# Kernel tuning notes

Measured on AMD Instinct MI355X. Metric: run time of the kernel, lower is better.

## Reference

```python
import jax, jax.numpy as jnp
import numpy as np

C = 64

def setup_inputs() -> dict:
    key = jax.random.key(0)
    ks = jax.random.split(key, 8)
    B, H, W = 4, 64, 64
    s = 1.0 / np.sqrt(C)
    return {
        "x": jax.random.normal(ks[0], (B, C, H, W), dtype=jnp.float32),
        "ln_g": jnp.ones((C,), jnp.float32),
        "ln_b": jnp.zeros((C,), jnp.float32),
        "wq": jax.random.normal(ks[1], (C, C), jnp.float32) * s,
        "bq": jnp.zeros((C,), jnp.float32),
        "wk": jax.random.normal(ks[2], (C, 1, 3, 3), jnp.float32) / 3.0,
        "bk": jnp.zeros((C,), jnp.float32),
        "wv": jax.random.normal(ks[3], (C, 1, 3, 3), jnp.float32) / 3.0,
        "bv": jnp.zeros((C,), jnp.float32),
        "wo": jax.random.normal(ks[4], (C, C), jnp.float32) * s,
        "bo": jnp.zeros((C,), jnp.float32),
    }

def _dwconv3x3(x, w, b):
    # depthwise 3x3, padding=1, groups=C; x: (B,C,H,W), w: (C,1,3,3)
    y = jax.lax.conv_general_dilated(
        x, w, window_strides=(1, 1), padding="SAME",
        feature_group_count=x.shape[1],
        dimension_numbers=("NCHW", "OIHW", "NCHW"))
    return y + b[None, :, None, None]

def reference(x, ln_g, ln_b, wq, bq, wk, bk, wv, bv, wo, bo):
    B, Cc, H, W = x.shape
    scale = jnp.sqrt(jnp.asarray(Cc, x.dtype))
    # LayerNorm over channel dim (torch LayerNorm([C]) on (B,H,W,C))
    mu = jnp.mean(x, axis=1, keepdims=True)
    var = jnp.mean(jnp.square(x - mu), axis=1, keepdims=True)
    xn = (x - mu) / jnp.sqrt(var + 1e-5)
    xn = xn * ln_g[None, :, None, None] + ln_b[None, :, None, None]
    # projections
    q = jnp.einsum("oc,bchw->bohw", wq, xn) + bq[None, :, None, None]
    k = _dwconv3x3(xn, wk, bk)
    v = _dwconv3x3(xn, wv, bv)
    HW = H * W
    qf = q.reshape(B, Cc, HW)  # (B,C,N)
    kf = k.reshape(B, Cc, HW)
    vf = v.reshape(B, Cc, HW)
    # attn[b,i,j] = sum_c q[b,c,i] k[b,c,j] / sqrt(C)
    attn = jnp.einsum("bci,bcj->bij", qf, kf) / scale
    attn = jax.nn.softmax(attn, axis=-1)
    # out[b,c,i] = sum_j attn[b,i,j] v[b,c,j]
    out = jnp.einsum("bij,bcj->bci", attn, vf).reshape(B, Cc, H, W)
    out = jnp.einsum("oc,bchw->bohw", wo, out) + bo[None, :, None, None]
    return out + x
```

## Files before the change

kernel.cpp:

```cpp
#include <hip/hip_runtime.h>
#include <stdint.h>

typedef __attribute__((ext_vector_type(8))) short short8;
typedef __attribute__((ext_vector_type(4))) float f32x4;

#define MFMA16(A, B, C) __builtin_amdgcn_mfma_f32_16x16x32_bf16(A, B, C, 0, 0, 0)

__device__ __forceinline__ short f2bf(float f) {
    uint32_t u = __float_as_uint(f);
    u = (u + 0x7fffu + ((u >> 16) & 1u)) >> 16;
    return (short)u;
}
__device__ __forceinline__ uint32_t pk_bf_trunc(float a, float b) {
    return __builtin_amdgcn_perm(__float_as_uint(b), __float_as_uint(a), 0x07060302u);
}
union PFU { uint32_t u[4]; short8 s; };

__device__ __forceinline__ void async_cp16(void* lds, const void* gm) {
    __builtin_amdgcn_global_load_lds(
        (const __attribute__((address_space(1))) unsigned int*)gm,
        (__attribute__((address_space(3))) unsigned int*)lds,
        16, 0, 0);
}

__device__ __forceinline__ int swz(int row, int col) {
    return row * 64 + ((((col >> 3) ^ (row & 7)) << 3) | (col & 7));
}
__device__ __forceinline__ int pimap(int j) {
    return ((j >> 5) << 5) + (((j >> 2) & 3) << 3) + (((j >> 4) & 1) << 2) + (j & 3);
}

__device__ __forceinline__ short8 ldg_f8_bf(const float* __restrict__ p) {
    float4 a = *(const float4*)p;
    float4 b = *(const float4*)(p + 4);
    short8 r;
    r[0] = f2bf(a.x); r[1] = f2bf(a.y); r[2] = f2bf(a.z); r[3] = f2bf(a.w);
    r[4] = f2bf(b.x); r[5] = f2bf(b.y); r[6] = f2bf(b.z); r[7] = f2bf(b.w);
    return r;
}

__global__ __launch_bounds__(512, 2) void k_lnqkv(
    const float* __restrict__ xg, const float* __restrict__ lng, const float* __restrict__ lnb,
    const float* __restrict__ wq, const float* __restrict__ bq,
    const float* __restrict__ wkg, const float* __restrict__ bk,
    const float* __restrict__ wvg, const float* __restrict__ bv,
    short* __restrict__ Qt, short* __restrict__ KVg)
{
    const int t    = threadIdx.x;
    const int wv   = t >> 6;
    const int lane = t & 63;
    const int l15  = lane & 15;
    const int quad = lane >> 4;
    const int h    = blockIdx.x;
    const int b    = blockIdx.y;
    const int w    = t & 63;
    const int g    = t >> 6;

    __shared__ float xl[3 * 64 * 66];
    __shared__ float sfu[3072];
    __shared__ float wkl[576], wvl[576], bkl[64], bvl[64];
    __shared__ float muL[192], rsL[192];

    float rv[24];
    float s0 = 0.f, s1 = 0.f, s2 = 0.f, q0 = 0.f, q1 = 0.f, q2 = 0.f;
    #pragma unroll
    for (int k = 0; k < 24; ++k) {
        const int dy = k >> 3, c = g + 8 * (k & 7);
        const int hh = h + dy - 1;
        float v = 0.f;
        if (hh >= 0 && hh < 64) v = xg[((b * 64 + c) * 64 + hh) * 64 + w];
        rv[k] = v;
        if (k < 8)       { s0 += v; q0 = fmaf(v, v, q0); }
        else if (k < 16) { s1 += v; q1 = fmaf(v, v, q1); }
        else             { s2 += v; q2 = fmaf(v, v, q2); }
    }
    float lngv[8], lnbv[8];
    #pragma unroll
    for (int j = 0; j < 8; ++j) { lngv[j] = lng[g + 8 * j]; lnbv[j] = lnb[g + 8 * j]; }
    for (int idx = t; idx < 576; idx += 512) { wkl[idx] = wkg[idx]; wvl[idx] = wvg[idx]; }
    if (t < 64) { bkl[t] = bk[t]; bvl[t] = bv[t]; }
    #pragma unroll
    for (int k = 0; k < 24; ++k)
        xl[((k >> 3) * 64 + g + 8 * (k & 7)) * 66 + w] = rv[k];
    sfu[(0 * 8 + g) * 64 + w] = s0; sfu[(1 * 8 + g) * 64 + w] = s1; sfu[(2 * 8 + g) * 64 + w] = s2;
    sfu[1536 + (0 * 8 + g) * 64 + w] = q0; sfu[1536 + (1 * 8 + g) * 64 + w] = q1; sfu[1536 + (2 * 8 + g) * 64 + w] = q2;
    __syncthreads();

    if (t < 192) {
        int dy = t >> 6, ww = t & 63;
        float S = 0.f, SS = 0.f;
        #pragma unroll
        for (int gg = 0; gg < 8; ++gg) {
            S  += sfu[(dy * 8 + gg) * 64 + ww];
            SS += sfu[1536 + (dy * 8 + gg) * 64 + ww];
        }
        float mu  = S * (1.f / 64.f);
        float var = SS * (1.f / 64.f) - mu * mu;
        muL[t] = mu;
        rsL[t] = rsqrtf(var + 1e-5f);
    }
    __syncthreads();

    short* xnt = (short*)sfu;
    {
        float mua = muL[w], rsa = rsL[w];
        float mub = muL[64 + w], rsb = rsL[64 + w];
        float muc = muL[128 + w], rsc = rsL[128 + w];
        #pragma unroll
        for (int k = 0; k < 24; ++k) {
            int dy = k >> 3, c = g + 8 * (k & 7);
            int hh = h + dy - 1;
            float mu = (k < 8) ? mua : (k < 16) ? mub : muc;
            float rs = (k < 8) ? rsa : (k < 16) ? rsb : rsc;
            float v = (rv[k] - mu) * rs * lngv[k & 7] + lnbv[k & 7];
            if (hh < 0 || hh >= 64) v = 0.f;
            xl[(dy * 64 + c) * 66 + w] = v;
            if (dy == 1) xnt[w * 72 + c] = f2bf(v);
        }
    }
    __syncthreads();

    {
        const int tile = wv >> 1, half = wv & 1;
        short8 af[2];
        #pragma unroll
        for (int kc = 0; kc < 2; ++kc)
            af[kc] = *(const short8*)&xnt[(tile * 16 + l15) * 72 + kc * 32 + quad * 8];
        f32x4 acc[2];
        acc[0] = (f32x4){0.f, 0.f, 0.f, 0.f};
        acc[1] = (f32x4){0.f, 0.f, 0.f, 0.f};
        #pragma unroll
        for (int kc = 0; kc < 2; ++kc) {
            #pragma unroll
            for (int ntl = 0; ntl < 2; ++ntl) {
                int nt = half * 2 + ntl;
                short8 bf = ldg_f8_bf(&wq[(nt * 16 + l15) * 64 + kc * 32 + quad * 8]);
                acc[ntl] = MFMA16(af[kc], bf, acc[ntl]);
            }
        }
        const float c1 = 0.18033688011112042f;
        #pragma unroll
        for (int ntl = 0; ntl < 2; ++ntl) {
            int o = (half * 2 + ntl) * 16 + l15;
            float bqv = bq[o];
            #pragma unroll
            for (int r = 0; r < 4; ++r) {
                int ww = tile * 16 + quad * 4 + r;
                Qt[((b * 4096 + h * 64 + ww) << 6) + o] = f2bf((acc[ntl][r] + bqv) * c1);
            }
        }
    }
    __syncthreads();

    short* vt = (short*)sfu;
    {
        int c  = t & 63;
        int w0 = wv << 3;
        float wk9[9], wv9[9];
        #pragma unroll
        for (int q = 0; q < 9; ++q) { wk9[q] = wkl[c * 9 + q]; wv9[q] = wvl[c * 9 + q]; }
        float acck[8], accv[8];
        #pragma unroll
        for (int j = 0; j < 8; ++j) { acck[j] = bkl[c]; accv[j] = bvl[c]; }
        #pragma unroll
        for (int dy = 0; dy < 3; ++dy) {
            const float* row = &xl[(dy * 64 + c) * 66];
            float r[10];
            r[0] = (w0 == 0) ? 0.f : row[w0 - 1];
            #pragma unroll
            for (int j2 = 0; j2 < 4; ++j2) {
                float2 p2 = *(const float2*)&row[w0 + j2 * 2];
                r[1 + j2 * 2] = p2.x; r[2 + j2 * 2] = p2.y;
            }
            r[9] = (w0 == 56) ? 0.f : row[w0 + 8];
            #pragma unroll
            for (int j = 0; j < 8; ++j) {
                acck[j] += wk9[dy * 3] * r[j] + wk9[dy * 3 + 1] * r[j + 1] + wk9[dy * 3 + 2] * r[j + 2];
                accv[j] += wv9[dy * 3] * r[j] + wv9[dy * 3 + 1] * r[j + 1] + wv9[dy * 3 + 2] * r[j + 2];
            }
        }
        long tb = (long)(b * 64 + h) * 8192;
        #pragma unroll
        for (int j = 0; j < 8; ++j)
            KVg[tb + swz(w0 + j, c)] = f2bf(acck[j]);
        #pragma unroll
        for (int j = 0; j < 8; ++j)
            vt[c * 68 + pimap(w0 + j)] = f2bf(accv[j]);
    }
    __syncthreads();

    {
        long tb = (long)(b * 64 + h) * 8192 + 4096;
        #pragma unroll
        for (int it = 0; it < 2; ++it) {
            int grp = t + it * 512;
            int c = grp >> 4, s0c = (grp & 15) * 4;
            uint2 v = *(const uint2*)&vt[c * 68 + s0c];
            int dst = c * 64 + ((((s0c >> 3) ^ (c & 7)) << 3) | (s0c & 7));
            *(uint2*)&KVg[tb + dst] = v;
        }
    }
}

__global__ __launch_bounds__(128, 2) void k_attn(
    const short* __restrict__ Qt, const short* __restrict__ KVg,
    short* __restrict__ Ogb, float* __restrict__ Lg)
{
    const int t    = threadIdx.x;
    const int wv   = t >> 6;
    const int lane = t & 63;
    const int l15  = lane & 15;
    const int quad = lane >> 4;
    const int ti   = blockIdx.x;
    const int jp   = blockIdx.y;
    const int b    = blockIdx.z;
    const int iw   = ti * 64 + wv * 32;

    __shared__ short kvb0[8192];
    __shared__ short kvb1[8192];

    const short* kvg = KVg + ((long)b * 64 + jp * 16) * 8192;

    short8 qf[2][2];
    #pragma unroll
    for (int rs = 0; rs < 2; ++rs)
        #pragma unroll
        for (int kc = 0; kc < 2; ++kc)
            qf[rs][kc] = *(const short8*)&Qt[((b * 4096 + iw + rs * 16 + l15) << 6) + kc * 32 + quad * 8];

    f32x4 oacc[2][4];
    #pragma unroll
    for (int rs = 0; rs < 2; ++rs)
        #pragma unroll
        for (int cb = 0; cb < 4; ++cb) oacc[rs][cb] = (f32x4){0.f, 0.f, 0.f, 0.f};
    float Lp[2] = {0.f, 0.f};

    #pragma unroll
    for (int ii = 0; ii < 8; ++ii)
        async_cp16(kvb0 + (wv * 8 + ii) * 512, kvg + (wv * 8 + ii) * 512 + lane * 8);

    const int xr = l15 & 7;

    #pragma unroll 1
    for (int jt = 0; jt < 16; ++jt) {
        short* cur = (jt & 1) ? kvb1 : kvb0;
        short* nxt = (jt & 1) ? kvb0 : kvb1;
        asm volatile("s_waitcnt vmcnt(0)" ::: "memory");
        __syncthreads();
        if (jt < 15) {
            const short* gsrc = kvg + (jt + 1) * 8192;
            #pragma unroll
            for (int ii = 0; ii < 8; ++ii)
                async_cp16(nxt + (wv * 8 + ii) * 512, gsrc + (wv * 8 + ii) * 512 + lane * 8);
        }

        short8 kf[4][2], vf[4][2];
        #pragma unroll
        for (int mb = 0; mb < 4; ++mb) {
            int rbase = (mb * 16 + l15) * 64;
            #pragma unroll
            for (int kc = 0; kc < 2; ++kc) {
                int cc = ((kc * 4 + quad) ^ xr) << 3;
                kf[mb][kc] = *(const short8*)&cur[rbase + cc];
                vf[mb][kc] = *(const short8*)&cur[4096 + rbase + cc];
            }
        }

        #pragma unroll
        for (int rs = 0; rs < 2; ++rs) {
            f32x4 sacc[4];
            #pragma unroll
            for (int mb = 0; mb < 4; ++mb) sacc[mb] = (f32x4){0.f, 0.f, 0.f, 0.f};
            #pragma unroll
            for (int kc = 0; kc < 2; ++kc)
                #pragma unroll
                for (int mb = 0; mb < 4; ++mb)
                    sacc[mb] = MFMA16(kf[mb][kc], qf[rs][kc], sacc[mb]);

            PFU pf[2];
            #pragma unroll
            for (int mb = 0; mb < 4; ++mb) {
                float p0 = __builtin_amdgcn_exp2f(sacc[mb][0]);
                float p1 = __builtin_amdgcn_exp2f(sacc[mb][1]);
                float p2 = __builtin_amdgcn_exp2f(sacc[mb][2]);
                float p3 = __builtin_amdgcn_exp2f(sacc[mb][3]);
                Lp[rs] += (p0 + p1) + (p2 + p3);
                pf[mb >> 1].u[(mb & 1) * 2 + 0] = pk_bf_trunc(p0, p1);
                pf[mb >> 1].u[(mb & 1) * 2 + 1] = pk_bf_trunc(p2, p3);
            }
            #pragma unroll
            for (int kcp = 0; kcp < 2; ++kcp)
                #pragma unroll
                for (int cb = 0; cb < 4; ++cb)
                    oacc[rs][cb] = MFMA16(vf[cb][kcp], pf[kcp].s, oacc[rs][cb]);
        }
    }

    const int p = b * 4 + jp;
    #pragma unroll
    for (int rs = 0; rs < 2; ++rs) {
        float L = Lp[rs];
        L += __shfl_xor(L, 16);
        L += __shfl_xor(L, 32);
        int i = iw + rs * 16 + l15;
        if (quad == 0) Lg[p * 4096 + i] = L;
        #pragma unroll
        for (int cb = 0; cb < 4; ++cb) {
            uint2 pk;
            pk.x = ((uint32_t)(uint16_t)f2bf(oacc[rs][cb][1]) << 16) | (uint16_t)f2bf(oacc[rs][cb][0]);
            pk.y = ((uint32_t)(uint16_t)f2bf(oacc[rs][cb][3]) << 16) | (uint16_t)f2bf(oacc[rs][cb][2]);
            *(uint2*)&Ogb[((p * 4096 + i) << 6) + cb * 16 + quad * 4] = pk;
        }
    }
}

__global__ __launch_bounds__(256, 4) void k_out(
    const short* __restrict__ Ogb, const float* __restrict__ Lg,
    const float* __restrict__ wo, const float* __restrict__ bo,
    const float* __restrict__ xg, float* __restrict__ out)
{
    const int t    = threadIdx.x;
    const int wv4  = t >> 6;
    const int lane = t & 63;
    const int l15  = lane & 15;
    const int quad = lane >> 4;
    const int i0   = blockIdx.x * 16;
    const int b    = blockIdx.y;

    float Ls = 0.f;
    #pragma unroll
    for (int jp = 0; jp < 4; ++jp) Ls += Lg[(b * 4 + jp) * 4096 + i0 + l15];
    float invL = 1.0f / Ls;

    short8 af[2];
    #pragma unroll
    for (int kc = 0; kc < 2; ++kc)
        af[kc] = ldg_f8_bf(&wo[(wv4 * 16 + l15) * 64 + kc * 32 + quad * 8]);

    f32x4 acc = (f32x4){0.f, 0.f, 0.f, 0.f};
    #pragma unroll
    for (int jp = 0; jp < 4; ++jp) {
        const short* obase = &Ogb[(((b * 4 + jp) * 4096 + i0 + l15) << 6) + quad * 8];
        #pragma unroll
        for (int kc = 0; kc < 2; ++kc) {
            short8 bfr = *(const short8*)&obase[kc * 32];
            acc = MFMA16(af[kc], bfr, acc);
        }
    }
    #pragma unroll
    for (int r = 0; r < 4; ++r) {
        int o = wv4 * 16 + quad * 4 + r;
        long obase = ((long)(b * 64 + o)) << 12;
        out[obase + i0 + l15] = acc[r] * invL + bo[o] + xg[obase + i0 + l15];
    }
}

extern "C" void kernel_launch(void* const* d_in, const int* in_sizes, int n_in,
                              void* d_out, int out_size, void* d_ws, size_t ws_size,
                              hipStream_t stream) {
    (void)in_sizes; (void)n_in; (void)out_size; (void)ws_size;
    const float* x   = (const float*)d_in[0];
    const float* lng = (const float*)d_in[1];
    const float* lnb = (const float*)d_in[2];
    const float* wq  = (const float*)d_in[3];
    const float* bq  = (const float*)d_in[4];
    const float* wk  = (const float*)d_in[5];
    const float* bk  = (const float*)d_in[6];
    const float* wvw = (const float*)d_in[7];
    const float* bv  = (const float*)d_in[8];
    const float* wo  = (const float*)d_in[9];
    const float* bo  = (const float*)d_in[10];
    float* out = (float*)d_out;

    short* Qt  = (short*)d_ws;
    short* KVg = Qt + 4 * 4096 * 64;
    short* Ogb = KVg + 4 * 64 * 8192;
    float* Lg  = (float*)(Ogb + 16 * 4096 * 64);

    k_lnqkv<<<dim3(64, 4), 512, 0, stream>>>(x, lng, lnb, wq, bq, wk, bk, wvw, bv, Qt, KVg);
    k_attn<<<dim3(64, 4, 4), 128, 0, stream>>>(Qt, KVg, Ogb, Lg);
    k_out<<<dim3(256, 4), 256, 0, stream>>>(Ogb, Lg, wo, bo, x, out);
}
```

Measured before the change: 113.9 us.

## Split attention work across four waves per block and remove a barrier in LN-QKV

The attention kernel now launches 256 threads per block, and each wave handles 16 query rows instead of 32. This halves the per-wave Q fragments and accumulators. K and V fragment loads are split into separate scoped phases to lower register pressure, and launch bounds are raised to target more resident waves. The LN/QKV kernel gets a dedicated LDS buffer for the V transpose, so the barrier that guarded reuse of the shared scratch can be dropped. The trade-off is that each block re-reads K/V tiles from LDS for fewer query rows, which lowers LDS reuse per MFMA.

Result: slower. 116.4 us (+2.2%).

```diff
diff --git a/kernel.cpp b/kernel.cpp
--- a/kernel.cpp
+++ b/kernel.cpp
@@ -58,6 +58,7 @@
 
     __shared__ float xl[3 * 64 * 66];
     __shared__ float sfu[3072];
+    __shared__ short vtb[64 * 68];
     __shared__ float wkl[576], wvl[576], bkl[64], bvl[64];
     __shared__ float muL[192], rsL[192];
 
@@ -150,9 +151,7 @@
             }
         }
     }
-    __syncthreads();
-
-    short* vt = (short*)sfu;
+
     {
         int c  = t & 63;
         int w0 = wv << 3;
@@ -185,7 +184,7 @@
             KVg[tb + swz(w0 + j, c)] = f2bf(acck[j]);
         #pragma unroll
         for (int j = 0; j < 8; ++j)
-            vt[c * 68 + pimap(w0 + j)] = f2bf(accv[j]);
+            vtb[c * 68 + pimap(w0 + j)] = f2bf(accv[j]);
     }
     __syncthreads();
 
@@ -195,14 +194,14 @@
         for (int it = 0; it < 2; ++it) {
             int grp = t + it * 512;
             int c = grp >> 4, s0c = (grp & 15) * 4;
-            uint2 v = *(const uint2*)&vt[c * 68 + s0c];
+            uint2 v = *(const uint2*)&vtb[c * 68 + s0c];
             int dst = c * 64 + ((((s0c >> 3) ^ (c & 7)) << 3) | (s0c & 7));
             *(uint2*)&KVg[tb + dst] = v;
         }
     }
 }
 
-__global__ __launch_bounds__(128, 2) void k_attn(
+__global__ __launch_bounds__(256, 4) void k_attn(
     const short* __restrict__ Qt, const short* __restrict__ KVg,
     short* __restrict__ Ogb, float* __restrict__ Lg)
 {
@@ -214,30 +213,26 @@
     const int ti   = blockIdx.x;
     const int jp   = blockIdx.y;
     const int b    = blockIdx.z;
-    const int iw   = ti * 64 + wv * 32;
+    const int iw   = ti * 64 + wv * 16;
 
     __shared__ short kvb0[8192];
     __shared__ short kvb1[8192];
 
     const short* kvg = KVg + ((long)b * 64 + jp * 16) * 8192;
 
-    short8 qf[2][2];
-    #pragma unroll
-    for (int rs = 0; rs < 2; ++rs)
-        #pragma unroll
-        for (int kc = 0; kc < 2; ++kc)
-            qf[rs][kc] = *(const short8*)&Qt[((b * 4096 + iw + rs * 16 + l15) << 6) + kc * 32 + quad * 8];
-
-    f32x4 oacc[2][4];
-    #pragma unroll
-    for (int rs = 0; rs < 2; ++rs)
-        #pragma unroll
-        for (int cb = 0; cb < 4; ++cb) oacc[rs][cb] = (f32x4){0.f, 0.f, 0.f, 0.f};
-    float Lp[2] = {0.f, 0.f};
-
-    #pragma unroll
-    for (int ii = 0; ii < 8; ++ii)
-        async_cp16(kvb0 + (wv * 8 + ii) * 512, kvg + (wv * 8 + ii) * 512 + lane * 8);
+    short8 qf[2];
+    #pragma unroll
+    for (int kc = 0; kc < 2; ++kc)
+        qf[kc] = *(const short8*)&Qt[((b * 4096 + iw + l15) << 6) + kc * 32 + quad * 8];
+
+    f32x4 oacc[4];
+    #pragma unroll
+    for (int cb = 0; cb < 4; ++cb) oacc[cb] = (f32x4){0.f, 0.f, 0.f, 0.f};
+    float Lp = 0.f;
+
+    #pragma unroll
+    for (int ii = 0; ii < 4; ++ii)
+        async_cp16(kvb0 + (wv * 4 + ii) * 512, kvg + (wv * 4 + ii) * 512 + lane * 8);
 
     const int xr = l15 & 7;
 
@@ -250,65 +245,70 @@
         if (jt < 15) {
             const short* gsrc = kvg + (jt + 1) * 8192;
             #pragma unroll
-            for (int ii = 0; ii < 8; ++ii)
-                async_cp16(nxt + (wv * 8 + ii) * 512, gsrc + (wv * 8 + ii) * 512 + lane * 8);
-        }
-
-        short8 kf[4][2], vf[4][2];
-        #pragma unroll
-        for (int mb = 0; mb < 4; ++mb) {
-            int rbase = (mb * 16 + l15) * 64;
-            #pragma unroll
-            for (int kc = 0; kc < 2; ++kc) {
-                int cc = ((kc * 4 + quad) ^ xr) << 3;
-                kf[mb][kc] = *(const short8*)&cur[rbase + cc];
-                vf[mb][kc] = *(const short8*)&cur[4096 + rbase + cc];
-            }
-        }
-
-        #pragma unroll
-        for (int rs = 0; rs < 2; ++rs) {
-            f32x4 sacc[4];
+            for (int ii = 0; ii < 4; ++ii)
+                async_cp16(nxt + (wv * 4 + ii) * 512, gsrc + (wv * 4 + ii) * 512 + lane * 8);
+        }
+
+        f32x4 sacc[4];
+        {
+            short8 kf[4][2];
+            #pragma unroll
+            for (int mb = 0; mb < 4; ++mb) {
+                int rbase = (mb * 16 + l15) * 64;
+                #pragma unroll
+                for (int kc = 0; kc < 2; ++kc)
+                    kf[mb][kc] = *(const short8*)&cur[rbase + (((kc * 4 + quad) ^ xr) << 3)];
+            }
             #pragma unroll
             for (int mb = 0; mb < 4; ++mb) sacc[mb] = (f32x4){0.f, 0.f, 0.f, 0.f};
             #pragma unroll
             for (int kc = 0; kc < 2; ++kc)
                 #pragma unroll
                 for (int mb = 0; mb < 4; ++mb)
-                    sacc[mb] = MFMA16(kf[mb][kc], qf[rs][kc], sacc[mb]);
-
-            PFU pf[2];
-            #pragma unroll
-            for (int mb = 0; mb < 4; ++mb) {
-                float p0 = __builtin_amdgcn_exp2f(sacc[mb][0]);
-                float p1 = __builtin_amdgcn_exp2f(sacc[mb][1]);
-                float p2 = __builtin_amdgcn_exp2f(sacc[mb][2]);
-                float p3 = __builtin_amdgcn_exp2f(sacc[mb][3]);
-                Lp[rs] += (p0 + p1) + (p2 + p3);
-                pf[mb >> 1].u[(mb & 1) * 2 + 0] = pk_bf_trunc(p0, p1);
-                pf[mb >> 1].u[(mb & 1) * 2 + 1] = pk_bf_trunc(p2, p3);
+                    sacc[mb] = MFMA16(kf[mb][kc], qf[kc], sacc[mb]);
+        }
+
+        PFU pf[2];
+        #pragma unroll
+        for (int mb = 0; mb < 4; ++mb) {
+            float p0 = __builtin_amdgcn_exp2f(sacc[mb][0]);
+            float p1 = __builtin_amdgcn_exp2f(sacc[mb][1]);
+            float p2 = __builtin_amdgcn_exp2f(sacc[mb][2]);
+            float p3 = __builtin_amdgcn_exp2f(sacc[mb][3]);
+            Lp += (p0 + p1) + (p2 + p3);
+            pf[mb >> 1].u[(mb & 1) * 2 + 0] = pk_bf_trunc(p0, p1);
+            pf[mb >> 1].u[(mb & 1) * 2 + 1] = pk_bf_trunc(p2, p3);
+        }
+
+        {
+            short8 vf[4][2];
+            #pragma unroll
+            for (int cb = 0; cb < 4; ++cb) {
+                int rbase = (cb * 16 + l15) * 64;
+                #pragma unroll
+                for (int kc = 0; kc < 2; ++kc)
+                    vf[cb][kc] = *(const short8*)&cur[4096 + rbase + (((kc * 4 + quad) ^ xr) << 3)];
             }
             #pragma unroll
             for (int kcp = 0; kcp < 2; ++kcp)
                 #pragma unroll
                 for (int cb = 0; cb < 4; ++cb)
-                    oacc[rs][cb] = MFMA16(vf[cb][kcp], pf[kcp].s, oacc[rs][cb]);
+                    oacc[cb] = MFMA16(vf[cb][kcp], pf[kcp].s, oacc[cb]);
         }
     }
 
     const int p = b * 4 + jp;
-    #pragma unroll
-    for (int rs = 0; rs < 2; ++rs) {
-        float L = Lp[rs];
+    {
+        float L = Lp;
         L += __shfl_xor(L, 16);
         L += __shfl_xor(L, 32);
-        int i = iw + rs * 16 + l15;
+        int i = iw + l15;
         if (quad == 0) Lg[p * 4096 + i] = L;
         #pragma unroll
         for (int cb = 0; cb < 4; ++cb) {
             uint2 pk;
-            pk.x = ((uint32_t)(uint16_t)f2bf(oacc[rs][cb][1]) << 16) | (uint16_t)f2bf(oacc[rs][cb][0]);
-            pk.y = ((uint32_t)(uint16_t)f2bf(oacc[rs][cb][3]) << 16) | (uint16_t)f2bf(oacc[rs][cb][2]);
+            pk.x = ((uint32_t)(uint16_t)f2bf(oacc[cb][1]) << 16) | (uint16_t)f2bf(oacc[cb][0]);
+            pk.y = ((uint32_t)(uint16_t)f2bf(oacc[cb][3]) << 16) | (uint16_t)f2bf(oacc[cb][2]);
             *(uint2*)&Ogb[((p * 4096 + i) << 6) + cb * 16 + quad * 4] = pk;
         }
     }
@@ -378,6 +378,6 @@
     float* Lg  = (float*)(Ogb + 16 * 4096 * 64);
 
     k_lnqkv<<<dim3(64, 4), 512, 0, stream>>>(x, lng, lnb, wq, bq, wk, bk, wvw, bv, Qt, KVg);
-    k_attn<<<dim3(64, 4, 4), 128, 0, stream>>>(Qt, KVg, Ogb, Lg);
+    k_attn<<<dim3(64, 4, 4), 256, 0, stream>>>(Qt, KVg, Ogb, Lg);
     k_out<<<dim3(256, 4), 256, 0, stream>>>(Ogb, Lg, wo, bo, x, out);
 }
```
